# Kernel tuning notes

Hardware: AMD Instinct MI355X
Metric: run time of the kernel (lower is better)

Reference implementation:

```python
import jax, jax.numpy as jnp
import numpy as np

EMBED = 1024
HEADS = 16
HEAD_DIM = EMBED // HEADS
B, T = 2, 2048
ROPE_THETA = 10000.0


def _rope(x):
    # x: [B, H, T, D]; standard half-split rotary embedding, applied per head
    D = x.shape[-1]
    inv_freq = 1.0 / (ROPE_THETA ** (jnp.arange(0, D, 2, dtype=jnp.float32) / D))  # [D/2]
    freqs = jnp.arange(x.shape[2], dtype=jnp.float32)[:, None] * inv_freq[None, :]  # [T, D/2]
    cos = jnp.cos(freqs).astype(x.dtype)  # [T, D/2]
    sin = jnp.sin(freqs).astype(x.dtype)
    x1, x2 = x[..., : D // 2], x[..., D // 2 :]
    return jnp.concatenate([x1 * cos - x2 * sin, x2 * cos + x1 * sin], axis=-1)


def setup_inputs() -> dict:
    key = jax.random.key(0)
    ks = jax.random.split(key, 5)
    s = 1.0 / np.sqrt(EMBED)
    return {
        "x": jax.random.normal(ks[0], (B, T, EMBED), dtype=jnp.float32),
        "Wq": jax.random.normal(ks[1], (EMBED, EMBED), dtype=jnp.float32) * s,
        "bq": jnp.zeros((EMBED,), dtype=jnp.float32),
        "Wk": jax.random.normal(ks[2], (EMBED, EMBED), dtype=jnp.float32) * s,
        "bk": jnp.zeros((EMBED,), dtype=jnp.float32),
        "Wv": jax.random.normal(ks[3], (EMBED, EMBED), dtype=jnp.float32) * s,
        "bv": jnp.zeros((EMBED,), dtype=jnp.float32),
        "Wo": jax.random.normal(ks[4], (EMBED, EMBED), dtype=jnp.float32) * s,
        "bo": jnp.zeros((EMBED,), dtype=jnp.float32),
    }


def reference(x, Wq, bq, Wk, bk, Wv, bv, Wo, bo):
    Bb, Tt, C = x.shape
    H, D = HEADS, HEAD_DIM
    # torch Linear: y = x @ W.T + b
    def proj(W, b):
        return (jnp.einsum("btc,oc->bto", x, W) + b).reshape(Bb, Tt, H, D).transpose(0, 2, 1, 3)

    q = _rope(proj(Wq, bq))  # [B, H, T, D]
    k = _rope(proj(Wk, bk))
    v = proj(Wv, bv)
    scale = jnp.sqrt(jnp.asarray(D, dtype=x.dtype))
    scores = jnp.einsum("bhtd,bhsd->bhts", q, k) / scale  # [B, H, T, T]
    attn = jax.nn.softmax(scores, axis=-1)  # dropout = identity in eval mode
    out = jnp.einsum("bhts,bhsd->bhtd", attn, v)  # [B, H, T, D]
    out = out.transpose(0, 2, 1, 3).reshape(Bb, Tt, C)
    return jnp.einsum("btc,oc->bto", out, Wo) + bo
```

## Files before the change

kernel.cpp:

```cpp
#include <hip/hip_runtime.h>
#include <hip/hip_bf16.h>

#define EMBED 1024
#define HEADS 16
#define HDIM 64
#define BATCH 2
#define SEQ 2048
#define MTOT (BATCH*SEQ)

typedef __attribute__((ext_vector_type(2))) float f32x2;
typedef __attribute__((ext_vector_type(4))) float f32x4;
typedef __attribute__((ext_vector_type(16))) float f32x16;
typedef __attribute__((ext_vector_type(4))) short s16x4;
typedef __attribute__((ext_vector_type(8))) short bf16x8;
typedef __attribute__((ext_vector_type(4))) int i32x4;

static __device__ __forceinline__ short f2bf(float f) {
  unsigned u = __builtin_bit_cast(unsigned, f);
  unsigned r = (u + 0x7fffu + ((u >> 16) & 1u)) >> 16;
  return (short)r;
}
static __device__ __forceinline__ float bf2f(short s) {
  unsigned u = ((unsigned)(unsigned short)s) << 16;
  return __builtin_bit_cast(float, u);
}
static __device__ __forceinline__ int pack2bf_fast(float lo, float hi) {
  unsigned ulo = __builtin_bit_cast(unsigned, lo) + 0x8000u;
  unsigned uhi = __builtin_bit_cast(unsigned, hi) + 0x8000u;
  int r;
  asm("v_cvt_pk_bf16_f32 %0, %1, %2" : "=v"(r)
      : "v"(__builtin_bit_cast(float, ulo)), "v"(__builtin_bit_cast(float, uhi)));
  return r;
}
static __device__ __forceinline__ void pswap(int &a, int &b) {
  asm("v_permlane32_swap_b32 %0, %1" : "+v"(a), "+v"(b));
}

typedef __attribute__((address_space(1))) const void gvoid_t;
typedef __attribute__((address_space(3))) void lvoid_t;
static __device__ __forceinline__ void gload_lds16(const void* g, void* l) {
  __builtin_amdgcn_global_load_lds((gvoid_t*)g, (lvoid_t*)l, 16, 0, 0);
}

__global__ __launch_bounds__(256) void cvt_bf16(
    const float* __restrict__ x,
    const float* __restrict__ Wq, const float* __restrict__ Wk,
    const float* __restrict__ Wv, const float* __restrict__ Wo,
    short* __restrict__ xb,
    short* __restrict__ Wqb, short* __restrict__ Wkb,
    short* __restrict__ Wvb, short* __restrict__ Wob,
    f32x2* __restrict__ tab)
{
  int i = blockIdx.x * 256 + threadIdx.x;
  if (i >= 2097152) {
    int i2 = i - 2097152;
    int t = i2 >> 5, j = i2 & 31;
    float invf = exp2f(-(float)j * 0.4152410118609203f);
    float sn, cs;
    sincosf((float)t * invf, &sn, &cs);
    f32x2 e; e[0] = cs; e[1] = sn;
    tab[i2] = e;
    return;
  }
  const float* src; short* dst; int off;
  if (i < 1048576) { src = x; dst = xb; off = i; }
  else {
    int j = i - 1048576;
    int w = j >> 18; off = j & 262143;
    src = (w == 0) ? Wq : (w == 1) ? Wk : (w == 2) ? Wv : Wo;
    dst = (w == 0) ? Wqb : (w == 1) ? Wkb : (w == 2) ? Wvb : Wob;
  }
  f32x4 v = ((const f32x4*)src)[off];
  s16x4 h;
#pragma unroll
  for (int j = 0; j < 4; ++j) h[j] = f2bf(v[j]);
  ((s16x4*)dst)[off] = h;
}

__global__ __launch_bounds__(256) void qkv_gemm(
    const short* __restrict__ xb,
    const short* __restrict__ Wqb, const short* __restrict__ Wkb, const short* __restrict__ Wvb,
    const float* __restrict__ bq, const float* __restrict__ bk, const float* __restrict__ bv,
    const f32x2* __restrict__ tab,
    short* __restrict__ Qb, short* __restrict__ Kb, short* __restrict__ Vb)
{
  __shared__ short As[128][64];
  __shared__ short Bs[128][64];
  int tid = threadIdx.x;
  int lane = tid & 63, wid = tid >> 6;
  int wm = wid >> 1, wn = wid & 1;
  int bm = blockIdx.x / 24;
  int bncol = blockIdx.x % 24;
  int wsel = bncol >> 3, bnn = bncol & 7;
  const short* W    = (wsel == 0) ? Wqb : (wsel == 1) ? Wkb : Wvb;
  const float* bias = (wsel == 0) ? bq : (wsel == 1) ? bk : bv;

  f32x4 acc[4][4] = {};

  const short* Abase = xb + (size_t)bm * 128 * EMBED;
  const short* Bbase = W + (size_t)bnn * 128 * EMBED;
  char* AsB = (char*)&As[0][0];
  char* BsB = (char*)&Bs[0][0];

  for (int kt = 0; kt < EMBED / 64; ++kt) {
#pragma unroll
    for (int i = 0; i < 4; ++i) {
      int s = tid + i * 256;
      int row = s >> 3, c = s & 7;
      int cs = c ^ (row & 7);
      gload_lds16(&Abase[(size_t)row * EMBED + kt * 64 + cs * 8],
                  AsB + i * 4096 + wid * 1024 + lane * 16);
      gload_lds16(&Bbase[(size_t)row * EMBED + kt * 64 + cs * 8],
                  BsB + i * 4096 + wid * 1024 + lane * 16);
    }
    __syncthreads();
#pragma unroll
    for (int kk = 0; kk < 2; ++kk) {
      int cp = ((kk * 4 + (lane >> 4)) ^ (lane & 7)) * 8;
      bf16x8 af[4], bfr[4];
#pragma unroll
      for (int mf = 0; mf < 4; ++mf)
        af[mf] = *(const bf16x8*)&As[wm * 64 + mf * 16 + (lane & 15)][cp];
#pragma unroll
      for (int nf = 0; nf < 4; ++nf)
        bfr[nf] = *(const bf16x8*)&Bs[wn * 64 + nf * 16 + (lane & 15)][cp];
      if (wsel == 2) {
#pragma unroll
        for (int mf = 0; mf < 4; ++mf)
#pragma unroll
          for (int nf = 0; nf < 4; ++nf)
            acc[mf][nf] = __builtin_amdgcn_mfma_f32_16x16x32_bf16(bfr[mf], af[nf], acc[mf][nf], 0, 0, 0);
      } else {
#pragma unroll
        for (int mf = 0; mf < 4; ++mf)
#pragma unroll
          for (int nf = 0; nf < 4; ++nf)
            acc[mf][nf] = __builtin_amdgcn_mfma_f32_16x16x32_bf16(af[mf], bfr[nf], acc[mf][nf], 0, 0, 0);
      }
    }
    __syncthreads();
  }

  if (wsel < 2) {
    short* dst = (wsel == 0) ? Qb : Kb;
    float sc = (wsel == 0) ? 0.18033688011112042f : 1.0f;
#pragma unroll
    for (int nf = 0; nf < 2; ++nf) {
      int col = bnn * 128 + wn * 64 + nf * 16 + (lane & 15);
      int h = col >> 6, j = col & 31;
      float b1 = bias[col], b2 = bias[col + 32];
#pragma unroll
      for (int mf = 0; mf < 4; ++mf) {
        int row0 = bm * 128 + wm * 64 + mf * 16 + ((lane >> 4) << 2);
#pragma unroll
        for (int r = 0; r < 4; ++r) {
          int m = row0 + r;
          int b_ = m >> 11, t = m & (SEQ - 1);
          f32x2 e = tab[t * 32 + j];
          float a1 = acc[mf][nf][r] + b1;
          float a2 = acc[mf][nf + 2][r] + b2;
          size_t o = (((size_t)(b_ * HEADS + h)) * SEQ + t) * HDIM + j;
          dst[o]      = f2bf((a1 * e[0] - a2 * e[1]) * sc);
          dst[o + 32] = f2bf((a2 * e[0] + a1 * e[1]) * sc);
        }
      }
    }
  } else {
#pragma unroll
    for (int mf = 0; mf < 4; ++mf) {
#pragma unroll
      for (int r = 0; r < 4; ++r) {
        int cch = bnn * 128 + wn * 64 + mf * 16 + ((lane >> 4) << 2) + r;
        int h = cch >> 6, d = cch & 63;
        float bb = bias[cch];
#pragma unroll
        for (int nf = 0; nf < 4; ++nf) {
          int m = bm * 128 + wm * 64 + nf * 16 + (lane & 15);
          int b_ = m >> 11, t = m & (SEQ - 1);
          Vb[((size_t)(b_ * HEADS + h) * HDIM + d) * SEQ + t] = f2bf(acc[mf][nf][r] + bb);
        }
      }
    }
  }
}

#define QBLK 128
#define KBLK 64

__global__ __launch_bounds__(256, 2) void attn_kernel(
    const short* __restrict__ Qb, const short* __restrict__ Kb,
    const short* __restrict__ Vb, short* __restrict__ Ob)
{
  __shared__ short Ks[2][KBLK][68];
  __shared__ short Vs[2][HDIM][68];

  int tid = threadIdx.x, lane = tid & 63, wid = tid >> 6;
  int l31 = lane & 31, lhi = lane >> 5;

  int bid = blockIdx.x;
  int swz = (bid & 7) * 64 + (bid >> 3);
  int qi = swz & 15, bh = swz >> 4;
  int b = bh >> 4, h = bh & 15;

  const short* Qp = Qb + ((size_t)bh * SEQ + qi * QBLK + wid * 32) * HDIM;
  const short* Kp = Kb + (size_t)bh * SEQ * HDIM;
  const short* Vp = Vb + (size_t)bh * HDIM * SEQ;

  bf16x8 qf[4];
#pragma unroll
  for (int cc = 0; cc < 4; ++cc)
    qf[cc] = *(const bf16x8*)&Qp[(size_t)l31 * HDIM + cc * 16 + lhi * 8];

  f32x16 oacc0 = {}, oacc1 = {}, lacc = {};
  bf16x8 vones;
#pragma unroll
  for (int j = 0; j < 8; ++j) vones[j] = (short)0x3F80;

  bf16x8 kreg[2], vreg[2];
#pragma unroll
  for (int i = 0; i < 2; ++i) {
    int s = tid + i * 256;
    kreg[i] = *(const bf16x8*)&Kp[(size_t)(s >> 3) * HDIM + (s & 7) * 8];
    vreg[i] = *(const bf16x8*)&Vp[(size_t)(s >> 3) * SEQ + (s & 7) * 8];
  }
#pragma unroll
  for (int i = 0; i < 2; ++i) {
    int s = tid + i * 256;
    *(bf16x8*)&Ks[0][s >> 3][(s & 7) * 8] = kreg[i];
    *(bf16x8*)&Vs[0][s >> 3][(s & 7) * 8] = vreg[i];
  }
  __syncthreads();

  for (int kt = 0; kt < SEQ / KBLK; ++kt) {
    int cur = kt & 1;
    if (kt + 1 < SEQ / KBLK) {
#pragma unroll
      for (int i = 0; i < 2; ++i) {
        int s = tid + i * 256;
        kreg[i] = *(const bf16x8*)&Kp[(size_t)((kt + 1) * KBLK + (s >> 3)) * HDIM + (s & 7) * 8];
        vreg[i] = *(const bf16x8*)&Vp[(size_t)(s >> 3) * SEQ + (kt + 1) * KBLK + (s & 7) * 8];
      }
    }

    f32x16 s0 = {}, s1 = {};
#pragma unroll
    for (int cc = 0; cc < 4; ++cc) {
      bf16x8 a0 = *(const bf16x8*)&Ks[cur][l31][cc * 16 + lhi * 8];
      bf16x8 a1 = *(const bf16x8*)&Ks[cur][32 + l31][cc * 16 + lhi * 8];
      s0 = __builtin_amdgcn_mfma_f32_32x32x16_bf16(a0, qf[cc], s0, 0, 0, 0);
      s1 = __builtin_amdgcn_mfma_f32_32x32x16_bf16(a1, qf[cc], s1, 0, 0, 0);
    }
    f32x16 p0, p1;
#pragma unroll
    for (int i = 0; i < 16; ++i) {
      p0[i] = __builtin_amdgcn_exp2f(s0[i]);
      p1[i] = __builtin_amdgcn_exp2f(s1[i]);
    }

#pragma unroll
    for (int c = 0; c < 2; ++c) {
      int w0 = pack2bf_fast(p0[8 * c + 0], p0[8 * c + 1]);
      int w1 = pack2bf_fast(p0[8 * c + 2], p0[8 * c + 3]);
      int w2 = pack2bf_fast(p0[8 * c + 4], p0[8 * c + 5]);
      int w3 = pack2bf_fast(p0[8 * c + 6], p0[8 * c + 7]);
      pswap(w0, w2);
      pswap(w1, w3);
      i32x4 pw; pw[0] = w0; pw[1] = w1; pw[2] = w2; pw[3] = w3;
      bf16x8 pa = __builtin_bit_cast(bf16x8, pw);

      bf16x8 vf0 = *(const bf16x8*)&Vs[cur][l31][c * 16 + lhi * 8];
      bf16x8 vf1 = *(const bf16x8*)&Vs[cur][32 + l31][c * 16 + lhi * 8];
      lacc = __builtin_amdgcn_mfma_f32_32x32x16_bf16(pa, vones, lacc, 0, 0, 0);
      oacc0 = __builtin_amdgcn_mfma_f32_32x32x16_bf16(pa, vf0, oacc0, 0, 0, 0);
      oacc1 = __builtin_amdgcn_mfma_f32_32x32x16_bf16(pa, vf1, oacc1, 0, 0, 0);
    }
#pragma unroll
    for (int c = 0; c < 2; ++c) {
      int w0 = pack2bf_fast(p1[8 * c + 0], p1[8 * c + 1]);
      int w1 = pack2bf_fast(p1[8 * c + 2], p1[8 * c + 3]);
      int w2 = pack2bf_fast(p1[8 * c + 4], p1[8 * c + 5]);
      int w3 = pack2bf_fast(p1[8 * c + 6], p1[8 * c + 7]);
      pswap(w0, w2);
      pswap(w1, w3);
      i32x4 pw; pw[0] = w0; pw[1] = w1; pw[2] = w2; pw[3] = w3;
      bf16x8 pa = __builtin_bit_cast(bf16x8, pw);

      bf16x8 vf0 = *(const bf16x8*)&Vs[cur][l31][32 + c * 16 + lhi * 8];
      bf16x8 vf1 = *(const bf16x8*)&Vs[cur][32 + l31][32 + c * 16 + lhi * 8];
      lacc = __builtin_amdgcn_mfma_f32_32x32x16_bf16(pa, vones, lacc, 0, 0, 0);
      oacc0 = __builtin_amdgcn_mfma_f32_32x32x16_bf16(pa, vf0, oacc0, 0, 0, 0);
      oacc1 = __builtin_amdgcn_mfma_f32_32x32x16_bf16(pa, vf1, oacc1, 0, 0, 0);
    }

    if (kt + 1 < SEQ / KBLK) {
#pragma unroll
      for (int i = 0; i < 2; ++i) {
        int s = tid + i * 256;
        *(bf16x8*)&Ks[cur ^ 1][s >> 3][(s & 7) * 8] = kreg[i];
        *(bf16x8*)&Vs[cur ^ 1][s >> 3][(s & 7) * 8] = vreg[i];
      }
      __syncthreads();
    }
  }

#pragma unroll
  for (int r = 0; r < 16; ++r) {
    int qrow = (r & 3) + 8 * (r >> 2) + 4 * lhi;
    int t = qi * QBLK + wid * 32 + qrow;
    float inv = 1.0f / lacc[r];
    size_t base = ((size_t)(b * SEQ + t)) * EMBED + h * HDIM;
    Ob[base + l31]      = f2bf(oacc0[r] * inv);
    Ob[base + 32 + l31] = f2bf(oacc1[r] * inv);
  }
}

__global__ __launch_bounds__(256) void out_gemm(
    const short* __restrict__ A, const short* __restrict__ Wob,
    const float* __restrict__ bo, float* __restrict__ C)
{
  __shared__ short As[2][64][64];
  __shared__ short Bs[2][128][64];
  int tid = threadIdx.x;
  int lane = tid & 63, wid = tid >> 6;
  int bm = blockIdx.x >> 3, bn = blockIdx.x & 7;

  f32x4 acc[8] = {};
  const short* Abase = A + (size_t)bm * 64 * EMBED;
  const short* Bbase = Wob + (size_t)bn * 128 * EMBED;
  char* AsB = (char*)&As[0][0][0];
  char* BsB = (char*)&Bs[0][0][0];
  const int ATSZ = 64 * 64 * 2;
  const int BTSZ = 128 * 64 * 2;

#pragma unroll
  for (int i = 0; i < 2; ++i) {
    int s = tid + i * 256;
    int row = s >> 3, c = s & 7;
    int cs = c ^ (row & 7);
    gload_lds16(&Abase[(size_t)row * EMBED + cs * 8],
                AsB + i * 4096 + wid * 1024 + lane * 16);
  }
#pragma unroll
  for (int i = 0; i < 4; ++i) {
    int s = tid + i * 256;
    int row = s >> 3, c = s & 7;
    int cs = c ^ (row & 7);
    gload_lds16(&Bbase[(size_t)row * EMBED + cs * 8],
                BsB + i * 4096 + wid * 1024 + lane * 16);
  }
  __syncthreads();

  for (int kt = 0; kt < EMBED / 64; ++kt) {
    int cur = kt & 1;
    if (kt + 1 < EMBED / 64) {
#pragma unroll
      for (int i = 0; i < 2; ++i) {
        int s = tid + i * 256;
        int row = s >> 3, c = s & 7;
        int cs = c ^ (row & 7);
        gload_lds16(&Abase[(size_t)row * EMBED + (kt + 1) * 64 + cs * 8],
                    AsB + (cur ^ 1) * ATSZ + i * 4096 + wid * 1024 + lane * 16);
      }
#pragma unroll
      for (int i = 0; i < 4; ++i) {
        int s = tid + i * 256;
        int row = s >> 3, c = s & 7;
        int cs = c ^ (row & 7);
        gload_lds16(&Bbase[(size_t)row * EMBED + (kt + 1) * 64 + cs * 8],
                    BsB + (cur ^ 1) * BTSZ + i * 4096 + wid * 1024 + lane * 16);
      }
    }

#pragma unroll
    for (int kk = 0; kk < 2; ++kk) {
      int cp = ((kk * 4 + (lane >> 4)) ^ (lane & 7)) * 8;
      bf16x8 af = *(const bf16x8*)&As[cur][wid * 16 + (lane & 15)][cp];
#pragma unroll
      for (int nf = 0; nf < 8; ++nf) {
        bf16x8 bfr = *(const bf16x8*)&Bs[cur][nf * 16 + (lane & 15)][cp];
        acc[nf] = __builtin_amdgcn_mfma_f32_16x16x32_bf16(af, bfr, acc[nf], 0, 0, 0);
      }
    }
    __syncthreads();
  }

#pragma unroll
  for (int nf = 0; nf < 8; ++nf) {
    int col = bn * 128 + nf * 16 + (lane & 15);
    float bb = bo[col];
    int row0 = bm * 64 + wid * 16 + ((lane >> 4) << 2);
#pragma unroll
    for (int r = 0; r < 4; ++r)
      C[(size_t)(row0 + r) * EMBED + col] = acc[nf][r] + bb;
  }
}

extern "C" void kernel_launch(void* const* d_in, const int* in_sizes, int n_in,
                              void* d_out, int out_size, void* d_ws, size_t ws_size,
                              hipStream_t stream) {
  const float* x  = (const float*)d_in[0];
  const float* Wq = (const float*)d_in[1];
  const float* bq = (const float*)d_in[2];
  const float* Wk = (const float*)d_in[3];
  const float* bk = (const float*)d_in[4];
  const float* Wv = (const float*)d_in[5];
  const float* bv = (const float*)d_in[6];
  const float* Wo = (const float*)d_in[7];
  const float* bo = (const float*)d_in[8];
  float* out = (float*)d_out;
  char* ws = (char*)d_ws;

  const size_t MB = 1u << 20;
  short* Qb  = (short*)(ws);
  short* Kb  = (short*)(ws + 8 * MB);
  short* Vb  = (short*)(ws + 16 * MB);
  short* XOb = (short*)(ws + 24 * MB);
  short* Wqb = (short*)(ws + 32 * MB);
  short* Wkb = (short*)(ws + 34 * MB);
  short* Wvb = (short*)(ws + 36 * MB);
  short* Wob = (short*)(ws + 38 * MB);
  f32x2* tab = (f32x2*)(ws + 40 * MB);

  cvt_bf16<<<dim3(8448), dim3(256), 0, stream>>>(x, Wq, Wk, Wv, Wo, XOb, Wqb, Wkb, Wvb, Wob, tab);
  qkv_gemm<<<dim3(32 * 24), dim3(256), 0, stream>>>(XOb, Wqb, Wkb, Wvb, bq, bk, bv, tab, Qb, Kb, Vb);
  attn_kernel<<<dim3(BATCH * HEADS * (SEQ / QBLK)), dim3(256), 0, stream>>>(Qb, Kb, Vb, XOb);
  out_gemm<<<dim3(64 * 8), dim3(256), 0, stream>>>(XOb, Wob, bo, out);
}
```

Measured before the change: 117.0 us.

## Split attention over two key halves with a combine pass; convert Wo inside out_gemm

The attention kernel now splits the key/value sequence into two halves, so twice as many blocks run. Each half writes a normalized partial output plus its row-sum, and a new combine kernel merges the two using the row-sums as weights. Separately, the fp32→bf16 conversion of Wo leaves the conversion kernel: out_gemm loads Wo as fp32 and packs it to bf16 in registers before storing to LDS. The trade is an extra kernel launch and partial-output traffic, against more attention parallelism and one less weight conversion pass.

```diff
diff --git a/kernel.cpp b/kernel.cpp
--- a/kernel.cpp
+++ b/kernel.cpp
@@ -45,15 +45,14 @@
 __global__ __launch_bounds__(256) void cvt_bf16(
     const float* __restrict__ x,
     const float* __restrict__ Wq, const float* __restrict__ Wk,
-    const float* __restrict__ Wv, const float* __restrict__ Wo,
+    const float* __restrict__ Wv,
     short* __restrict__ xb,
-    short* __restrict__ Wqb, short* __restrict__ Wkb,
-    short* __restrict__ Wvb, short* __restrict__ Wob,
+    short* __restrict__ Wqb, short* __restrict__ Wkb, short* __restrict__ Wvb,
     f32x2* __restrict__ tab)
 {
   int i = blockIdx.x * 256 + threadIdx.x;
-  if (i >= 2097152) {
-    int i2 = i - 2097152;
+  if (i >= 1835008) {
+    int i2 = i - 1835008;
     int t = i2 >> 5, j = i2 & 31;
     float invf = exp2f(-(float)j * 0.4152410118609203f);
     float sn, cs;
@@ -67,8 +66,8 @@
   else {
     int j = i - 1048576;
     int w = j >> 18; off = j & 262143;
-    src = (w == 0) ? Wq : (w == 1) ? Wk : (w == 2) ? Wv : Wo;
-    dst = (w == 0) ? Wqb : (w == 1) ? Wkb : (w == 2) ? Wvb : Wob;
+    src = (w == 0) ? Wq : (w == 1) ? Wk : Wv;
+    dst = (w == 0) ? Wqb : (w == 1) ? Wkb : Wvb;
   }
   f32x4 v = ((const f32x4*)src)[off];
   s16x4 h;
@@ -186,10 +185,13 @@
 
 #define QBLK 128
 #define KBLK 64
+#define KSPAN 1024
 
 __global__ __launch_bounds__(256, 2) void attn_kernel(
     const short* __restrict__ Qb, const short* __restrict__ Kb,
-    const short* __restrict__ Vb, short* __restrict__ Ob)
+    const short* __restrict__ Vb,
+    short* __restrict__ P0, short* __restrict__ P1,
+    float* __restrict__ L0, float* __restrict__ L1)
 {
   __shared__ short Ks[2][KBLK][68];
   __shared__ short Vs[2][HDIM][68];
@@ -198,13 +200,18 @@
   int l31 = lane & 31, lhi = lane >> 5;
 
   int bid = blockIdx.x;
-  int swz = (bid & 7) * 64 + (bid >> 3);
-  int qi = swz & 15, bh = swz >> 4;
+  int swz = (bid & 7) * 128 + (bid >> 3);
+  int kg = swz >> 9;
+  int rr = swz & 511;
+  int qi = rr & 15, bh = rr >> 4;
   int b = bh >> 4, h = bh & 15;
 
+  short* Op = kg ? P1 : P0;
+  float* Lp = kg ? L1 : L0;
+
   const short* Qp = Qb + ((size_t)bh * SEQ + qi * QBLK + wid * 32) * HDIM;
-  const short* Kp = Kb + (size_t)bh * SEQ * HDIM;
-  const short* Vp = Vb + (size_t)bh * HDIM * SEQ;
+  const short* Kp = Kb + ((size_t)bh * SEQ + kg * KSPAN) * HDIM;
+  const short* Vp = Vb + (size_t)bh * HDIM * SEQ + kg * KSPAN;
 
   bf16x8 qf[4];
 #pragma unroll
@@ -231,9 +238,9 @@
   }
   __syncthreads();
 
-  for (int kt = 0; kt < SEQ / KBLK; ++kt) {
+  for (int kt = 0; kt < KSPAN / KBLK; ++kt) {
     int cur = kt & 1;
-    if (kt + 1 < SEQ / KBLK) {
+    if (kt + 1 < KSPAN / KBLK) {
 #pragma unroll
       for (int i = 0; i < 2; ++i) {
         int s = tid + i * 256;
@@ -292,7 +299,7 @@
       oacc1 = __builtin_amdgcn_mfma_f32_32x32x16_bf16(pa, vf1, oacc1, 0, 0, 0);
     }
 
-    if (kt + 1 < SEQ / KBLK) {
+    if (kt + 1 < KSPAN / KBLK) {
 #pragma unroll
       for (int i = 0; i < 2; ++i) {
         int s = tid + i * 256;
@@ -309,13 +316,37 @@
     int t = qi * QBLK + wid * 32 + qrow;
     float inv = 1.0f / lacc[r];
     size_t base = ((size_t)(b * SEQ + t)) * EMBED + h * HDIM;
-    Ob[base + l31]      = f2bf(oacc0[r] * inv);
-    Ob[base + 32 + l31] = f2bf(oacc1[r] * inv);
-  }
+    Op[base + l31]      = f2bf(oacc0[r] * inv);
+    Op[base + 32 + l31] = f2bf(oacc1[r] * inv);
+    if (l31 == 0)
+      Lp[(size_t)bh * SEQ + t] = lacc[r];
+  }
+}
+
+__global__ __launch_bounds__(256) void combine_kernel(
+    const short* __restrict__ P0, const short* __restrict__ P1,
+    const float* __restrict__ L0, const float* __restrict__ L1,
+    short* __restrict__ O)
+{
+  int i = blockIdx.x * 256 + threadIdx.x;
+  int row64 = i >> 3, c8 = (i & 7) * 8;
+  int h = row64 & 15, bt = row64 >> 4;
+  int lidx = ((bt >> 11) * HEADS + h) * SEQ + (bt & (SEQ - 1));
+  float l0 = L0[lidx], l1 = L1[lidx];
+  float inv = 1.0f / (l0 + l1);
+  float w0 = l0 * inv, w1 = l1 * inv;
+  size_t base = (size_t)row64 * 64 + c8;
+  bf16x8 a = *(const bf16x8*)&P0[base];
+  bf16x8 bq = *(const bf16x8*)&P1[base];
+  bf16x8 o;
+#pragma unroll
+  for (int j = 0; j < 8; ++j)
+    o[j] = f2bf(bf2f(a[j]) * w0 + bf2f(bq[j]) * w1);
+  *(bf16x8*)&O[base] = o;
 }
 
 __global__ __launch_bounds__(256) void out_gemm(
-    const short* __restrict__ A, const short* __restrict__ Wob,
+    const short* __restrict__ A, const float* __restrict__ Wof,
     const float* __restrict__ bo, float* __restrict__ C)
 {
   __shared__ short As[2][64][64];
@@ -326,11 +357,13 @@
 
   f32x4 acc[8] = {};
   const short* Abase = A + (size_t)bm * 64 * EMBED;
-  const short* Bbase = Wob + (size_t)bn * 128 * EMBED;
+  const float* Bbase = Wof + (size_t)bn * 128 * EMBED;
   char* AsB = (char*)&As[0][0][0];
   char* BsB = (char*)&Bs[0][0][0];
   const int ATSZ = 64 * 64 * 2;
   const int BTSZ = 128 * 64 * 2;
+
+  f32x4 bregf[8];
 
 #pragma unroll
   for (int i = 0; i < 2; ++i) {
@@ -338,15 +371,22 @@
     int row = s >> 3, c = s & 7;
     int cs = c ^ (row & 7);
     gload_lds16(&Abase[(size_t)row * EMBED + cs * 8],
-                AsB + i * 4096 + wid * 1024 + lane * 16);
+                AsB + i * 4096 + tid * 16);
   }
 #pragma unroll
   for (int i = 0; i < 4; ++i) {
     int s = tid + i * 256;
     int row = s >> 3, c = s & 7;
     int cs = c ^ (row & 7);
-    gload_lds16(&Bbase[(size_t)row * EMBED + cs * 8],
-                BsB + i * 4096 + wid * 1024 + lane * 16);
+    const float* src = &Bbase[(size_t)row * EMBED + cs * 8];
+    f32x4 v0 = *(const f32x4*)src;
+    f32x4 v1 = *(const f32x4*)(src + 4);
+    i32x4 pw;
+    pw[0] = pack2bf_fast(v0[0], v0[1]);
+    pw[1] = pack2bf_fast(v0[2], v0[3]);
+    pw[2] = pack2bf_fast(v1[0], v1[1]);
+    pw[3] = pack2bf_fast(v1[2], v1[3]);
+    *(i32x4*)(BsB + i * 4096 + tid * 16) = pw;
   }
   __syncthreads();
 
@@ -359,15 +399,16 @@
         int row = s >> 3, c = s & 7;
         int cs = c ^ (row & 7);
         gload_lds16(&Abase[(size_t)row * EMBED + (kt + 1) * 64 + cs * 8],
-                    AsB + (cur ^ 1) * ATSZ + i * 4096 + wid * 1024 + lane * 16);
+                    AsB + (cur ^ 1) * ATSZ + i * 4096 + tid * 16);
       }
 #pragma unroll
       for (int i = 0; i < 4; ++i) {
         int s = tid + i * 256;
         int row = s >> 3, c = s & 7;
         int cs = c ^ (row & 7);
-        gload_lds16(&Bbase[(size_t)row * EMBED + (kt + 1) * 64 + cs * 8],
-                    BsB + (cur ^ 1) * BTSZ + i * 4096 + wid * 1024 + lane * 16);
+        const float* src = &Bbase[(size_t)row * EMBED + (kt + 1) * 64 + cs * 8];
+        bregf[2 * i]     = *(const f32x4*)src;
+        bregf[2 * i + 1] = *(const f32x4*)(src + 4);
       }
     }
 
@@ -381,7 +422,19 @@
         acc[nf] = __builtin_amdgcn_mfma_f32_16x16x32_bf16(af, bfr, acc[nf], 0, 0, 0);
       }
     }
-    __syncthreads();
+
+    if (kt + 1 < EMBED / 64) {
+#pragma unroll
+      for (int i = 0; i < 4; ++i) {
+        i32x4 pw;
+        pw[0] = pack2bf_fast(bregf[2 * i][0], bregf[2 * i][1]);
+        pw[1] = pack2bf_fast(bregf[2 * i][2], bregf[2 * i][3]);
+        pw[2] = pack2bf_fast(bregf[2 * i + 1][0], bregf[2 * i + 1][1]);
+        pw[3] = pack2bf_fast(bregf[2 * i + 1][2], bregf[2 * i + 1][3]);
+        *(i32x4*)(BsB + (cur ^ 1) * BTSZ + i * 4096 + tid * 16) = pw;
+      }
+      __syncthreads();
+    }
   }
 
 #pragma unroll
@@ -418,11 +471,15 @@
   short* Wqb = (short*)(ws + 32 * MB);
   short* Wkb = (short*)(ws + 34 * MB);
   short* Wvb = (short*)(ws + 36 * MB);
-  short* Wob = (short*)(ws + 38 * MB);
   f32x2* tab = (f32x2*)(ws + 40 * MB);
-
-  cvt_bf16<<<dim3(8448), dim3(256), 0, stream>>>(x, Wq, Wk, Wv, Wo, XOb, Wqb, Wkb, Wvb, Wob, tab);
+  short* P0  = XOb;
+  short* P1  = (short*)(ws + 32 * MB);
+  float* L0  = (float*)(ws + 40 * MB);
+  float* L1  = L0 + (size_t)BATCH * HEADS * SEQ;
+
+  cvt_bf16<<<dim3(7424), dim3(256), 0, stream>>>(x, Wq, Wk, Wv, XOb, Wqb, Wkb, Wvb, tab);
   qkv_gemm<<<dim3(32 * 24), dim3(256), 0, stream>>>(XOb, Wqb, Wkb, Wvb, bq, bk, bv, tab, Qb, Kb, Vb);
-  attn_kernel<<<dim3(BATCH * HEADS * (SEQ / QBLK)), dim3(256), 0, stream>>>(Qb, Kb, Vb, XOb);
-  out_gemm<<<dim3(64 * 8), dim3(256), 0, stream>>>(XOb, Wob, bo, out);
-}
+  attn_kernel<<<dim3(2 * BATCH * HEADS * (SEQ / QBLK)), dim3(256), 0, stream>>>(Qb, Kb, Vb, P0, P1, L0, L1);
+  combine_kernel<<<dim3(2048), dim3(256), 0, stream>>>(P0, P1, L0, L1, Qb);
+  out_gemm<<<dim3(64 * 8), dim3(256), 0, stream>>>(Qb, Wo, bo, out);
+}
```

After: 130.1 us. 11.2% more time.
